# Optimization experiments

Hardware: AMD Instinct MI355X
Metric: run time of the kernel (lower is better)

Reference implementation:

```python
import jax, jax.numpy as jnp
import numpy as np

B, QN, D_IN = 2, 2048, 1024
NDS = QN // 2
HEADS, DIM_HEAD = 16, 64
INNER = HEADS * DIM_HEAD  # 1024
D_OUT = 1024


def setup_inputs() -> dict:
    key = jax.random.key(0)
    ks = jax.random.split(key, 7)
    s = 0.02
    return {
        "unet_full": jax.random.normal(ks[0], (B, QN, D_IN), jnp.float32),
        "unet_downsampled": jax.random.normal(ks[1], (B, NDS, D_IN), jnp.float32),
        "Wq": jax.random.normal(ks[2], (D_IN, INNER), jnp.float32) * s,
        "Wk": jax.random.normal(ks[3], (D_IN, INNER), jnp.float32) * s,
        "Wv": jax.random.normal(ks[4], (D_IN, INNER), jnp.float32) * s,
        "Wo": jax.random.normal(ks[5], (INNER, D_OUT), jnp.float32) * s,
        "bo": jnp.zeros((D_OUT,), jnp.float32),
    }


def reference(unet_full, unet_downsampled, Wq, Wk, Wv, Wo, bo):
    # projections
    q = unet_full @ Wq                      # [B, QN, H*D]
    k = unet_downsampled @ Wk               # [B, NDS, H*D]
    v = unet_downsampled @ Wv
    # repeat kv along sequence dim (torch repeat(1,2,1) == tile twice on dim 1)
    k = jnp.concatenate([k, k], axis=1)     # [B, KVN=2*NDS, H*D]
    v = jnp.concatenate([v, v], axis=1)
    kvn = k.shape[1]
    # split heads
    q = q.reshape(B, QN, HEADS, DIM_HEAD)
    k = k.reshape(B, kvn, HEADS, DIM_HEAD)
    v = v.reshape(B, kvn, HEADS, DIM_HEAD)
    # banded mask: triu(diagonal=-2) keeps entries where j >= i - 2; log -> 0 allowed, -inf blocked
    i = jnp.arange(QN)[:, None]
    j = jnp.arange(kvn)[None, :]
    bias = jnp.where(j >= i - 2, 0.0, -jnp.inf).astype(q.dtype)  # [QN, KVN]
    scale = 1.0 / jnp.sqrt(jnp.asarray(DIM_HEAD, q.dtype))
    scores = jnp.einsum('bqhd,bkhd->bhqk', q, k) * scale + bias[None, None]
    attn = jax.nn.softmax(scores, axis=-1)
    out = jnp.einsum('bhqk,bkhd->bqhd', attn, v)  # [B, QN, H, D]
    out = out.reshape(B, QN, INNER)
    return out @ Wo + bo
```

## Files before the change

kernel.cpp:

```cpp
#include <hip/hip_runtime.h>

typedef __attribute__((ext_vector_type(8))) short short8;
typedef __attribute__((ext_vector_type(4))) short short4v;
typedef __attribute__((ext_vector_type(4))) float floatx4;
typedef __attribute__((ext_vector_type(4))) unsigned int uint4v;
typedef __attribute__((ext_vector_type(2))) unsigned int uint2v;

__device__ __forceinline__ unsigned short f2bf(float f) {
  unsigned u = __float_as_uint(f);
  u += 0x7FFFu + ((u >> 16) & 1u);
  return (unsigned short)(u >> 16);
}
__device__ __forceinline__ unsigned pack_bf2(float f0, float f1) {
  unsigned a = __float_as_uint(f0) + 0x8000u;
  unsigned b = __float_as_uint(f1) + 0x8000u;
  return __builtin_amdgcn_perm(b, a, 0x07060302u);
}
__device__ __forceinline__ void async16(const unsigned short* g, unsigned short* l) {
  __builtin_amdgcn_global_load_lds(
      (const __attribute__((address_space(1))) unsigned int*)g,
      (__attribute__((address_space(3))) unsigned int*)l, 16, 0, 0);
}

#define B_   2
#define QN_  2048
#define NDS_ 1024
#define H_   16
#define C_SC 0.18033688011f

__global__ __launch_bounds__(256) void prep(
    const float* __restrict__ Wq, const float* __restrict__ Wk,
    const float* __restrict__ Wv, const float* __restrict__ Wo,
    unsigned short* __restrict__ WT) {
  int bid = blockIdx.x;
  int z = bid >> 8, tile = bid & 255;
  const float* W = z == 0 ? Wq : z == 1 ? Wk : z == 2 ? Wv : Wo;
  unsigned short* out = WT + (size_t)z * (1u << 20);
  __shared__ unsigned short tilebuf[64][65];
  int bi = tile >> 4, bj = tile & 15;
  int c = threadIdx.x & 63, r0 = threadIdx.x >> 6;
#pragma unroll
  for (int i = 0; i < 64; i += 4)
    tilebuf[r0 + i][c] = f2bf(W[(size_t)(bi * 64 + r0 + i) * 1024 + bj * 64 + c]);
  __syncthreads();
#pragma unroll
  for (int i = 0; i < 64; i += 4)
    out[(size_t)(bj * 64 + r0 + i) * 1024 + bi * 64 + c] = tilebuf[c][r0 + i];
}

__global__ __launch_bounds__(512) void gemm_qkv(
    const float* __restrict__ full, const float* __restrict__ ds,
    const unsigned short* __restrict__ WT,
    unsigned short* __restrict__ Qb, unsigned short* __restrict__ Kb,
    unsigned short* __restrict__ Vt) {
  __shared__ __align__(16) unsigned short As[128 * 64];
  __shared__ __align__(16) unsigned short Bs[128 * 64];
  int t = threadIdx.x;
  int lane = t & 63, wave = t >> 6;
  int lrow = lane & 15, quad = lane >> 4;
  int by = blockIdx.x;
  int colBase = blockIdx.y * 128;
  int wr = (wave & 3) * 32, wc = (wave >> 2) * 64;
  int sw = lrow & 7;

  int sel = (by < 32) ? 0 : (by < 48 ? 1 : 2);
  const unsigned short* Wt = WT + (size_t)sel * (1u << 20);
  const float* Afp = (sel == 0) ? full : ds;
  size_t arow0 = (sel == 0) ? (size_t)by * 128
                            : (size_t)(by - (sel == 1 ? 32 : 48)) * 128;

  floatx4 acc[2][4];
#pragma unroll
  for (int mi = 0; mi < 2; ++mi)
#pragma unroll
    for (int ni = 0; ni < 4; ++ni) acc[mi][ni] = (floatx4){0.f, 0.f, 0.f, 0.f};

  for (int k0 = 0; k0 < 1024; k0 += 64) {
    __syncthreads();
#pragma unroll
    for (int it = 0; it < 2; ++it) {
      int linear = it * 512 + t;
      int row = linear >> 3;
      int cg = (linear & 7) ^ (row & 7);
      const float* p = Afp + (arow0 + row) * 1024 + k0 + cg * 8;
      floatx4 x = *(const floatx4*)p, y = *(const floatx4*)(p + 4);
      uint4v u = {pack_bf2(x[0], x[1]), pack_bf2(x[2], x[3]),
                  pack_bf2(y[0], y[1]), pack_bf2(y[2], y[3])};
      *(uint4v*)&As[linear * 8] = u;
      async16(Wt + (size_t)(colBase + row) * 1024 + k0 + cg * 8, Bs + linear * 8);
    }
    __syncthreads();

#pragma unroll
    for (int ks = 0; ks < 2; ++ks) {
      int fc = ((ks * 4 + quad) ^ sw) * 8;
      short8 af[2], bfr[4];
#pragma unroll
      for (int mi = 0; mi < 2; ++mi)
        af[mi] = *(const short8*)&As[(wr + mi * 16 + lrow) * 64 + fc];
#pragma unroll
      for (int ni = 0; ni < 4; ++ni)
        bfr[ni] = *(const short8*)&Bs[(wc + ni * 16 + lrow) * 64 + fc];
#pragma unroll
      for (int mi = 0; mi < 2; ++mi)
#pragma unroll
        for (int ni = 0; ni < 4; ++ni)
          acc[mi][ni] =
              __builtin_amdgcn_mfma_f32_16x16x32_bf16(af[mi], bfr[ni], acc[mi][ni], 0, 0, 0);
    }
  }

#pragma unroll
  for (int mi = 0; mi < 2; ++mi)
#pragma unroll
    for (int ni = 0; ni < 4; ++ni) {
      int col = colBase + wc + ni * 16 + lrow;
      if (sel == 2) {
        size_t r0g = arow0 + wr + mi * 16 + quad * 4;
        size_t b = r0g >> 10, kv = r0g & 1023;
        short4v pk;
#pragma unroll
        for (int r = 0; r < 4; ++r) pk[r] = (short)f2bf(acc[mi][ni][r]);
        *(short4v*)&Vt[b * (1u << 20) + (size_t)col * 1024 + kv] = pk;
      } else {
        unsigned short* C = (sel == 0) ? Qb : Kb;
#pragma unroll
        for (int r = 0; r < 4; ++r) {
          size_t row = arow0 + wr + mi * 16 + quad * 4 + r;
          C[row * 1024 + col] = f2bf(acc[mi][ni][r]);
        }
      }
    }
}

#define PSTR 40
__global__ __launch_bounds__(512) void attn_kernel(
    const unsigned short* __restrict__ Q,
    const unsigned short* __restrict__ K,
    const unsigned short* __restrict__ V,
    unsigned short* __restrict__ O) {
  __shared__ __align__(16) unsigned short Ks[2][32 * 64];
  __shared__ __align__(16) unsigned short Vs[2][64 * 32];
  __shared__ __align__(16) unsigned short Pl[8][16 * PSTR];
  int t = threadIdx.x, lane = t & 63, wave = t >> 6;
  int lrow = lane & 15, quad = lane >> 4;
  int bh = blockIdx.y, b = bh >> 4, h = bh & 15;
  int q0 = blockIdx.x * 128, qtile = q0 + wave * 16;
  int swk = lrow & 7, swv = (lrow >> 1) & 3;

  const unsigned short* qp =
      Q + (size_t)(b * QN_ + qtile + lrow) * 1024 + h * 64 + quad * 8;
  short8 qb0 = *(const short8*)qp;
  short8 qb1 = *(const short8*)(qp + 32);

  int ts = t & 255;
  int krow = ts >> 3, kq = (ts & 7) ^ (krow & 7);
  const unsigned short* ksrc =
      K + (size_t)(b * NDS_ + krow) * 1024 + h * 64 + kq * 8;
  int vrow = ts >> 2, vq = (ts & 3) ^ ((vrow >> 1) & 3);
  const unsigned short* vsrc =
      V + ((size_t)b * 1024 + h * 64 + vrow) * 1024 + vq * 8;

  int c0 = (q0 >= 1058) ? (((q0 - 1058) >> 5) + 1) : 0;
  if (t < 256) async16(ksrc + (size_t)c0 * 32 * 1024, &Ks[0][ts * 8]);
  else         async16(vsrc + c0 * 32, &Vs[0][ts * 8]);
  const unsigned short* kpre = ksrc + (size_t)(c0 + 1) * 32 * 1024;
  const unsigned short* vpre = vsrc + (c0 + 1) * 32;

  floatx4 acc_o[4];
#pragma unroll
  for (int dt = 0; dt < 4; ++dt) acc_o[dt] = (floatx4){0.f, 0.f, 0.f, 0.f};
  float den0 = 0.f, den1 = 0.f;
  int t1 = qtile + lrow - 2, t2 = qtile + lrow - 1026;
  unsigned short* P = Pl[wave];
  int buf = 0;

  for (int c = c0; c < 32; ++c) {
    __syncthreads();
    if (c + 1 < 32) {
      if (t < 256) async16(kpre, &Ks[buf ^ 1][ts * 8]);
      else         async16(vpre, &Vs[buf ^ 1][ts * 8]);
      kpre += 32 * 1024;
      vpre += 32;
    }
    int cb = c * 32;
    bool fast2 = (cb >= qtile + 13);
    bool fast1 = (cb <= qtile - 34) && (cb >= qtile - 1011);
    if (fast1 || fast2) {
      float bias = fast2 ? 1.f : 0.f;
#pragma unroll
      for (int nt = 0; nt < 2; ++nt) {
        const unsigned short* kb = &Ks[buf][(nt * 16 + lrow) * 64];
        short8 ka0 = *(const short8*)(kb + (quad ^ swk) * 8);
        short8 ka1 = *(const short8*)(kb + ((quad + 4) ^ swk) * 8);
        floatx4 z = (floatx4){0.f, 0.f, 0.f, 0.f};
        z = __builtin_amdgcn_mfma_f32_16x16x32_bf16(ka0, qb0, z, 0, 0, 0);
        z = __builtin_amdgcn_mfma_f32_16x16x32_bf16(ka1, qb1, z, 0, 0, 0);
        float p[4];
#pragma unroll
        for (int r = 0; r < 4; ++r) {
          p[r] = __builtin_amdgcn_exp2f(fmaf(z[r], C_SC, bias));
          if (nt == 0) den0 += p[r]; else den1 += p[r];
        }
        uint2v pw = {pack_bf2(p[0], p[1]), pack_bf2(p[2], p[3])};
        *(uint2v*)&P[lrow * PSTR + nt * 16 + quad * 4] = pw;
      }
    } else {
#pragma unroll
      for (int nt = 0; nt < 2; ++nt) {
        const unsigned short* kb = &Ks[buf][(nt * 16 + lrow) * 64];
        short8 ka0 = *(const short8*)(kb + (quad ^ swk) * 8);
        short8 ka1 = *(const short8*)(kb + ((quad + 4) ^ swk) * 8);
        floatx4 z = (floatx4){0.f, 0.f, 0.f, 0.f};
        z = __builtin_amdgcn_mfma_f32_16x16x32_bf16(ka0, qb0, z, 0, 0, 0);
        z = __builtin_amdgcn_mfma_f32_16x16x32_bf16(ka1, qb1, z, 0, 0, 0);
        float p[4];
#pragma unroll
        for (int r = 0; r < 4; ++r) {
          int j0 = cb + nt * 16 + quad * 4 + r;
          float m = (j0 >= t1 ? 1.f : 0.f) + (j0 >= t2 ? 1.f : 0.f);
          p[r] = m * __builtin_amdgcn_exp2f(z[r] * C_SC);
          if (nt == 0) den0 += p[r]; else den1 += p[r];
        }
        uint2v pw = {pack_bf2(p[0], p[1]), pack_bf2(p[2], p[3])};
        *(uint2v*)&P[lrow * PSTR + nt * 16 + quad * 4] = pw;
      }
    }
    short8 pa = *(const short8*)&P[lrow * PSTR + quad * 8];
#pragma unroll
    for (int dt = 0; dt < 4; ++dt) {
      short8 vf =
          *(const short8*)&Vs[buf][(dt * 16 + lrow) * 32 + (quad ^ swv) * 8];
      acc_o[dt] = __builtin_amdgcn_mfma_f32_16x16x32_bf16(pa, vf, acc_o[dt], 0, 0, 0);
    }
    buf ^= 1;
  }
  float denom = den0 + den1;
  denom += __shfl_xor(denom, 16);
  denom += __shfl_xor(denom, 32);
  float dd[4];
#pragma unroll
  for (int r = 0; r < 4; ++r) dd[r] = __shfl(denom, quad * 4 + r);
#pragma unroll
  for (int dt = 0; dt < 4; ++dt)
#pragma unroll
    for (int r = 0; r < 4; ++r) {
      int i = qtile + quad * 4 + r;
      int col = h * 64 + dt * 16 + lrow;
      O[(size_t)(b * QN_ + i) * 1024 + col] = f2bf(acc_o[dt][r] / dd[r]);
    }
}

__global__ __launch_bounds__(512) void gemm_o(
    const unsigned short* __restrict__ Ab, const unsigned short* __restrict__ WoT,
    const float* __restrict__ bo, float* __restrict__ out) {
  __shared__ __align__(16) unsigned short As[64 * 64];
  __shared__ __align__(16) unsigned short Bs[128 * 64];
  int t = threadIdx.x;
  int lane = t & 63, wave = t >> 6;
  int lrow = lane & 15, quad = lane >> 4;
  size_t rowBase = (size_t)blockIdx.x * 64;
  int colBase = blockIdx.y * 128;
  int wr = (wave & 1) * 32, wc = (wave >> 1) * 32;
  int sw = lrow & 7;

  floatx4 acc[2][2];
#pragma unroll
  for (int mi = 0; mi < 2; ++mi)
#pragma unroll
    for (int ni = 0; ni < 2; ++ni) acc[mi][ni] = (floatx4){0.f, 0.f, 0.f, 0.f};

  for (int k0 = 0; k0 < 1024; k0 += 64) {
    __syncthreads();
    {
      int row = t >> 3;
      int cg = (t & 7) ^ (row & 7);
      async16(Ab + (rowBase + row) * 1024 + k0 + cg * 8, As + t * 8);
    }
#pragma unroll
    for (int it = 0; it < 2; ++it) {
      int linear = it * 512 + t;
      int row = linear >> 3;
      int cg = (linear & 7) ^ (row & 7);
      async16(WoT + (size_t)(colBase + row) * 1024 + k0 + cg * 8, Bs + linear * 8);
    }
    __syncthreads();

#pragma unroll
    for (int ks = 0; ks < 2; ++ks) {
      int fc = ((ks * 4 + quad) ^ sw) * 8;
      short8 af[2], bfr[2];
#pragma unroll
      for (int mi = 0; mi < 2; ++mi)
        af[mi] = *(const short8*)&As[(wr + mi * 16 + lrow) * 64 + fc];
#pragma unroll
      for (int ni = 0; ni < 2; ++ni)
        bfr[ni] = *(const short8*)&Bs[(wc + ni * 16 + lrow) * 64 + fc];
#pragma unroll
      for (int mi = 0; mi < 2; ++mi)
#pragma unroll
        for (int ni = 0; ni < 2; ++ni)
          acc[mi][ni] =
              __builtin_amdgcn_mfma_f32_16x16x32_bf16(af[mi], bfr[ni], acc[mi][ni], 0, 0, 0);
    }
  }

#pragma unroll
  for (int mi = 0; mi < 2; ++mi)
#pragma unroll
    for (int ni = 0; ni < 2; ++ni) {
      int col = colBase + wc + ni * 16 + lrow;
      float badd = bo[col];
#pragma unroll
      for (int r = 0; r < 4; ++r) {
        size_t row = rowBase + wr + mi * 16 + quad * 4 + r;
        out[row * 1024 + col] = acc[mi][ni][r] + badd;
      }
    }
}

extern "C" void kernel_launch(void* const* d_in, const int* in_sizes, int n_in,
                              void* d_out, int out_size, void* d_ws, size_t ws_size,
                              hipStream_t stream) {
  const float* full = (const float*)d_in[0];
  const float* ds   = (const float*)d_in[1];
  const float* Wq   = (const float*)d_in[2];
  const float* Wk   = (const float*)d_in[3];
  const float* Wv   = (const float*)d_in[4];
  const float* Wo   = (const float*)d_in[5];
  const float* bo   = (const float*)d_in[6];
  float* out = (float*)d_out;

  unsigned short* ws = (unsigned short*)d_ws;
  unsigned short* Qb  = ws;
  unsigned short* Kb  = ws + (4u << 20);
  unsigned short* Vt  = ws + (6u << 20);
  unsigned short* Ab  = ws + (8u << 20);
  unsigned short* WT  = ws + (12u << 20);
  unsigned short* WoT = WT + 3u * (1u << 20);

  prep<<<1024, 256, 0, stream>>>(Wq, Wk, Wv, Wo, WT);
  gemm_qkv<<<dim3(64, 8), 512, 0, stream>>>(full, ds, WT, Qb, Kb, Vt);
  attn_kernel<<<dim3(QN_ / 128, B_ * H_), 512, 0, stream>>>(Qb, Kb, Vt, Ab);
  gemm_o<<<dim3(64, 8), 512, 0, stream>>>(Ab, WoT, bo, out);
}
```

Baseline: 163.9 us.

## Give each attention wave two query tiles to reuse K/V fragments

The attention block drops from 8 to 4 waves, and each wave now handles 32 query rows as two 16-row subtiles. K and V fragments read from LDS are shared across both subtiles, and every thread issues both the K and V async loads. A chunk-level skip jumps past KV chunks that lie entirely in the masked region for the wave. The cost is more registers per wave and fewer waves per block, which may lower latency hiding.

```diff
diff --git a/kernel.cpp b/kernel.cpp
--- a/kernel.cpp
+++ b/kernel.cpp
@@ -134,7 +134,7 @@
 }
 
 #define PSTR 40
-__global__ __launch_bounds__(512) void attn_kernel(
+__global__ __launch_bounds__(256) void attn_kernel(
     const unsigned short* __restrict__ Q,
     const unsigned short* __restrict__ K,
     const unsigned short* __restrict__ V,
@@ -145,110 +145,129 @@
   int t = threadIdx.x, lane = t & 63, wave = t >> 6;
   int lrow = lane & 15, quad = lane >> 4;
   int bh = blockIdx.y, b = bh >> 4, h = bh & 15;
-  int q0 = blockIdx.x * 128, qtile = q0 + wave * 16;
+  int q0 = blockIdx.x * 128, qtile = q0 + wave * 32;
   int swk = lrow & 7, swv = (lrow >> 1) & 3;
 
-  const unsigned short* qp =
-      Q + (size_t)(b * QN_ + qtile + lrow) * 1024 + h * 64 + quad * 8;
-  short8 qb0 = *(const short8*)qp;
-  short8 qb1 = *(const short8*)(qp + 32);
-
-  int ts = t & 255;
-  int krow = ts >> 3, kq = (ts & 7) ^ (krow & 7);
+  short8 qb[2][2];
+#pragma unroll
+  for (int mi = 0; mi < 2; ++mi) {
+    const unsigned short* qp =
+        Q + (size_t)(b * QN_ + qtile + mi * 16 + lrow) * 1024 + h * 64 + quad * 8;
+    qb[mi][0] = *(const short8*)qp;
+    qb[mi][1] = *(const short8*)(qp + 32);
+  }
+
+  int krow = t >> 3, kq = (t & 7) ^ (krow & 7);
   const unsigned short* ksrc =
       K + (size_t)(b * NDS_ + krow) * 1024 + h * 64 + kq * 8;
-  int vrow = ts >> 2, vq = (ts & 3) ^ ((vrow >> 1) & 3);
+  int vrow = t >> 2, vq = (t & 3) ^ ((vrow >> 1) & 3);
   const unsigned short* vsrc =
       V + ((size_t)b * 1024 + h * 64 + vrow) * 1024 + vq * 8;
 
   int c0 = (q0 >= 1058) ? (((q0 - 1058) >> 5) + 1) : 0;
-  if (t < 256) async16(ksrc + (size_t)c0 * 32 * 1024, &Ks[0][ts * 8]);
-  else         async16(vsrc + c0 * 32, &Vs[0][ts * 8]);
+  async16(ksrc + (size_t)c0 * 32 * 1024, &Ks[0][t * 8]);
+  async16(vsrc + c0 * 32, &Vs[0][t * 8]);
   const unsigned short* kpre = ksrc + (size_t)(c0 + 1) * 32 * 1024;
   const unsigned short* vpre = vsrc + (c0 + 1) * 32;
 
-  floatx4 acc_o[4];
-#pragma unroll
-  for (int dt = 0; dt < 4; ++dt) acc_o[dt] = (floatx4){0.f, 0.f, 0.f, 0.f};
-  float den0 = 0.f, den1 = 0.f;
-  int t1 = qtile + lrow - 2, t2 = qtile + lrow - 1026;
-  unsigned short* P = Pl[wave];
+  floatx4 acc_o[2][4];
+#pragma unroll
+  for (int mi = 0; mi < 2; ++mi)
+#pragma unroll
+    for (int dt = 0; dt < 4; ++dt) acc_o[mi][dt] = (floatx4){0.f, 0.f, 0.f, 0.f};
+  float den[2][2] = {{0.f, 0.f}, {0.f, 0.f}};
+  unsigned short* P0 = Pl[wave * 2];
+  unsigned short* P1 = Pl[wave * 2 + 1];
   int buf = 0;
 
   for (int c = c0; c < 32; ++c) {
     __syncthreads();
     if (c + 1 < 32) {
-      if (t < 256) async16(kpre, &Ks[buf ^ 1][ts * 8]);
-      else         async16(vpre, &Vs[buf ^ 1][ts * 8]);
+      async16(kpre, &Ks[buf ^ 1][t * 8]);
+      async16(vpre, &Vs[buf ^ 1][t * 8]);
       kpre += 32 * 1024;
       vpre += 32;
     }
     int cb = c * 32;
-    bool fast2 = (cb >= qtile + 13);
-    bool fast1 = (cb <= qtile - 34) && (cb >= qtile - 1011);
-    if (fast1 || fast2) {
-      float bias = fast2 ? 1.f : 0.f;
-#pragma unroll
-      for (int nt = 0; nt < 2; ++nt) {
-        const unsigned short* kb = &Ks[buf][(nt * 16 + lrow) * 64];
-        short8 ka0 = *(const short8*)(kb + (quad ^ swk) * 8);
-        short8 ka1 = *(const short8*)(kb + ((quad + 4) ^ swk) * 8);
-        floatx4 z = (floatx4){0.f, 0.f, 0.f, 0.f};
-        z = __builtin_amdgcn_mfma_f32_16x16x32_bf16(ka0, qb0, z, 0, 0, 0);
-        z = __builtin_amdgcn_mfma_f32_16x16x32_bf16(ka1, qb1, z, 0, 0, 0);
-        float p[4];
-#pragma unroll
-        for (int r = 0; r < 4; ++r) {
-          p[r] = __builtin_amdgcn_exp2f(fmaf(z[r], C_SC, bias));
-          if (nt == 0) den0 += p[r]; else den1 += p[r];
+    if (cb + 31 >= qtile - 1026) {
+#pragma unroll
+      for (int mi = 0; mi < 2; ++mi) {
+        int qm = qtile + mi * 16;
+        unsigned short* P = mi ? P1 : P0;
+        bool fast2 = (cb >= qm + 13);
+        bool fast1 = (cb <= qm - 34) && (cb >= qm - 1011);
+        if (fast1 || fast2) {
+          float bias = fast2 ? 1.f : 0.f;
+#pragma unroll
+          for (int nt = 0; nt < 2; ++nt) {
+            const unsigned short* kb = &Ks[buf][(nt * 16 + lrow) * 64];
+            short8 ka0 = *(const short8*)(kb + (quad ^ swk) * 8);
+            short8 ka1 = *(const short8*)(kb + ((quad + 4) ^ swk) * 8);
+            floatx4 z = (floatx4){0.f, 0.f, 0.f, 0.f};
+            z = __builtin_amdgcn_mfma_f32_16x16x32_bf16(ka0, qb[mi][0], z, 0, 0, 0);
+            z = __builtin_amdgcn_mfma_f32_16x16x32_bf16(ka1, qb[mi][1], z, 0, 0, 0);
+            float p[4];
+#pragma unroll
+            for (int r = 0; r < 4; ++r) {
+              p[r] = __builtin_amdgcn_exp2f(fmaf(z[r], C_SC, bias));
+              den[mi][nt] += p[r];
+            }
+            uint2v pw = {pack_bf2(p[0], p[1]), pack_bf2(p[2], p[3])};
+            *(uint2v*)&P[lrow * PSTR + nt * 16 + quad * 4] = pw;
+          }
+        } else {
+          int t1 = qm + lrow - 2, t2 = qm + lrow - 1026;
+#pragma unroll
+          for (int nt = 0; nt < 2; ++nt) {
+            const unsigned short* kb = &Ks[buf][(nt * 16 + lrow) * 64];
+            short8 ka0 = *(const short8*)(kb + (quad ^ swk) * 8);
+            short8 ka1 = *(const short8*)(kb + ((quad + 4) ^ swk) * 8);
+            floatx4 z = (floatx4){0.f, 0.f, 0.f, 0.f};
+            z = __builtin_amdgcn_mfma_f32_16x16x32_bf16(ka0, qb[mi][0], z, 0, 0, 0);
+            z = __builtin_amdgcn_mfma_f32_16x16x32_bf16(ka1, qb[mi][1], z, 0, 0, 0);
+            float p[4];
+#pragma unroll
+            for (int r = 0; r < 4; ++r) {
+              int j0 = cb + nt * 16 + quad * 4 + r;
+              float m = (j0 >= t1 ? 1.f : 0.f) + (j0 >= t2 ? 1.f : 0.f);
+              p[r] = m * __builtin_amdgcn_exp2f(z[r] * C_SC);
+              den[mi][nt] += p[r];
+            }
+            uint2v pw = {pack_bf2(p[0], p[1]), pack_bf2(p[2], p[3])};
+            *(uint2v*)&P[lrow * PSTR + nt * 16 + quad * 4] = pw;
+          }
         }
-        uint2v pw = {pack_bf2(p[0], p[1]), pack_bf2(p[2], p[3])};
-        *(uint2v*)&P[lrow * PSTR + nt * 16 + quad * 4] = pw;
-      }
-    } else {
-#pragma unroll
-      for (int nt = 0; nt < 2; ++nt) {
-        const unsigned short* kb = &Ks[buf][(nt * 16 + lrow) * 64];
-        short8 ka0 = *(const short8*)(kb + (quad ^ swk) * 8);
-        short8 ka1 = *(const short8*)(kb + ((quad + 4) ^ swk) * 8);
-        floatx4 z = (floatx4){0.f, 0.f, 0.f, 0.f};
-        z = __builtin_amdgcn_mfma_f32_16x16x32_bf16(ka0, qb0, z, 0, 0, 0);
-        z = __builtin_amdgcn_mfma_f32_16x16x32_bf16(ka1, qb1, z, 0, 0, 0);
-        float p[4];
-#pragma unroll
-        for (int r = 0; r < 4; ++r) {
-          int j0 = cb + nt * 16 + quad * 4 + r;
-          float m = (j0 >= t1 ? 1.f : 0.f) + (j0 >= t2 ? 1.f : 0.f);
-          p[r] = m * __builtin_amdgcn_exp2f(z[r] * C_SC);
-          if (nt == 0) den0 += p[r]; else den1 += p[r];
-        }
-        uint2v pw = {pack_bf2(p[0], p[1]), pack_bf2(p[2], p[3])};
-        *(uint2v*)&P[lrow * PSTR + nt * 16 + quad * 4] = pw;
-      }
-    }
-    short8 pa = *(const short8*)&P[lrow * PSTR + quad * 8];
-#pragma unroll
-    for (int dt = 0; dt < 4; ++dt) {
-      short8 vf =
-          *(const short8*)&Vs[buf][(dt * 16 + lrow) * 32 + (quad ^ swv) * 8];
-      acc_o[dt] = __builtin_amdgcn_mfma_f32_16x16x32_bf16(pa, vf, acc_o[dt], 0, 0, 0);
+      }
+      short8 pa0 = *(const short8*)&P0[lrow * PSTR + quad * 8];
+      short8 pa1 = *(const short8*)&P1[lrow * PSTR + quad * 8];
+#pragma unroll
+      for (int dt = 0; dt < 4; ++dt) {
+        short8 vf =
+            *(const short8*)&Vs[buf][(dt * 16 + lrow) * 32 + (quad ^ swv) * 8];
+        acc_o[0][dt] = __builtin_amdgcn_mfma_f32_16x16x32_bf16(pa0, vf, acc_o[0][dt], 0, 0, 0);
+        acc_o[1][dt] = __builtin_amdgcn_mfma_f32_16x16x32_bf16(pa1, vf, acc_o[1][dt], 0, 0, 0);
+      }
     }
     buf ^= 1;
   }
-  float denom = den0 + den1;
-  denom += __shfl_xor(denom, 16);
-  denom += __shfl_xor(denom, 32);
-  float dd[4];
-#pragma unroll
-  for (int r = 0; r < 4; ++r) dd[r] = __shfl(denom, quad * 4 + r);
-#pragma unroll
-  for (int dt = 0; dt < 4; ++dt)
-#pragma unroll
-    for (int r = 0; r < 4; ++r) {
-      int i = qtile + quad * 4 + r;
-      int col = h * 64 + dt * 16 + lrow;
-      O[(size_t)(b * QN_ + i) * 1024 + col] = f2bf(acc_o[dt][r] / dd[r]);
-    }
+
+#pragma unroll
+  for (int mi = 0; mi < 2; ++mi) {
+    float denom = den[mi][0] + den[mi][1];
+    denom += __shfl_xor(denom, 16);
+    denom += __shfl_xor(denom, 32);
+    float dd[4];
+#pragma unroll
+    for (int r = 0; r < 4; ++r) dd[r] = __shfl(denom, quad * 4 + r);
+#pragma unroll
+    for (int dt = 0; dt < 4; ++dt)
+#pragma unroll
+      for (int r = 0; r < 4; ++r) {
+        int i = qtile + mi * 16 + quad * 4 + r;
+        int col = h * 64 + dt * 16 + lrow;
+        O[(size_t)(b * QN_ + i) * 1024 + col] = f2bf(acc_o[mi][dt][r] / dd[r]);
+      }
+  }
 }
 
 __global__ __launch_bounds__(512) void gemm_o(
@@ -341,6 +360,6 @@
 
   prep<<<1024, 256, 0, stream>>>(Wq, Wk, Wv, Wo, WT);
   gemm_qkv<<<dim3(64, 8), 512, 0, stream>>>(full, ds, WT, Qb, Kb, Vt);
-  attn_kernel<<<dim3(QN_ / 128, B_ * H_), 512, 0, stream>>>(Qb, Kb, Vt, Ab);
+  attn_kernel<<<dim3(QN_ / 128, B_ * H_), 256, 0, stream>>>(Qb, Kb, Vt, Ab);
   gemm_o<<<dim3(64, 8), 512, 0, stream>>>(Ab, WoT, bo, out);
 }
```

After: 180.7 us. +10.3%, slower.

## Load K/V fragments directly from global memory per wave, dropping LDS staging

Applied to the files above, without the earlier changes.

The attention kernel no longer stages K and V tiles in double-buffered shared memory with async loads and block-wide barriers. Each wave now reads its MFMA operands straight from global memory, relying on L1/L2 for reuse across the 8 waves. Each wave also computes its own starting chunk, so waves skip masked chunks independently. This removes the __syncthreads per chunk and the LDS traffic, but gives up the explicit prefetch and means eight redundant global loads per tile, which depends on cache hit rates.

```diff
diff --git a/kernel.cpp b/kernel.cpp
--- a/kernel.cpp
+++ b/kernel.cpp
@@ -139,33 +139,20 @@
     const unsigned short* __restrict__ K,
     const unsigned short* __restrict__ V,
     unsigned short* __restrict__ O) {
-  __shared__ __align__(16) unsigned short Ks[2][32 * 64];
-  __shared__ __align__(16) unsigned short Vs[2][64 * 32];
   __shared__ __align__(16) unsigned short Pl[8][16 * PSTR];
   int t = threadIdx.x, lane = t & 63, wave = t >> 6;
   int lrow = lane & 15, quad = lane >> 4;
   int bh = blockIdx.y, b = bh >> 4, h = bh & 15;
   int q0 = blockIdx.x * 128, qtile = q0 + wave * 16;
-  int swk = lrow & 7, swv = (lrow >> 1) & 3;
 
   const unsigned short* qp =
       Q + (size_t)(b * QN_ + qtile + lrow) * 1024 + h * 64 + quad * 8;
   short8 qb0 = *(const short8*)qp;
   short8 qb1 = *(const short8*)(qp + 32);
 
-  int ts = t & 255;
-  int krow = ts >> 3, kq = (ts & 7) ^ (krow & 7);
-  const unsigned short* ksrc =
-      K + (size_t)(b * NDS_ + krow) * 1024 + h * 64 + kq * 8;
-  int vrow = ts >> 2, vq = (ts & 3) ^ ((vrow >> 1) & 3);
-  const unsigned short* vsrc =
-      V + ((size_t)b * 1024 + h * 64 + vrow) * 1024 + vq * 8;
-
-  int c0 = (q0 >= 1058) ? (((q0 - 1058) >> 5) + 1) : 0;
-  if (t < 256) async16(ksrc + (size_t)c0 * 32 * 1024, &Ks[0][ts * 8]);
-  else         async16(vsrc + c0 * 32, &Vs[0][ts * 8]);
-  const unsigned short* kpre = ksrc + (size_t)(c0 + 1) * 32 * 1024;
-  const unsigned short* vpre = vsrc + (c0 + 1) * 32;
+  const unsigned short* Kb0 = K + (size_t)b * NDS_ * 1024 + h * 64 + quad * 8;
+  const unsigned short* Vb0 =
+      V + ((size_t)b * 1024 + h * 64 + lrow) * 1024 + quad * 8;
 
   floatx4 acc_o[4];
 #pragma unroll
@@ -173,16 +160,10 @@
   float den0 = 0.f, den1 = 0.f;
   int t1 = qtile + lrow - 2, t2 = qtile + lrow - 1026;
   unsigned short* P = Pl[wave];
-  int buf = 0;
-
-  for (int c = c0; c < 32; ++c) {
-    __syncthreads();
-    if (c + 1 < 32) {
-      if (t < 256) async16(kpre, &Ks[buf ^ 1][ts * 8]);
-      else         async16(vpre, &Vs[buf ^ 1][ts * 8]);
-      kpre += 32 * 1024;
-      vpre += 32;
-    }
+
+  int c0w = (qtile >= 1058) ? (((qtile - 1058) >> 5) + 1) : 0;
+
+  for (int c = c0w; c < 32; ++c) {
     int cb = c * 32;
     bool fast2 = (cb >= qtile + 13);
     bool fast1 = (cb <= qtile - 34) && (cb >= qtile - 1011);
@@ -190,9 +171,9 @@
       float bias = fast2 ? 1.f : 0.f;
 #pragma unroll
       for (int nt = 0; nt < 2; ++nt) {
-        const unsigned short* kb = &Ks[buf][(nt * 16 + lrow) * 64];
-        short8 ka0 = *(const short8*)(kb + (quad ^ swk) * 8);
-        short8 ka1 = *(const short8*)(kb + ((quad + 4) ^ swk) * 8);
+        const unsigned short* kr = Kb0 + (size_t)(cb + nt * 16 + lrow) * 1024;
+        short8 ka0 = *(const short8*)kr;
+        short8 ka1 = *(const short8*)(kr + 32);
         floatx4 z = (floatx4){0.f, 0.f, 0.f, 0.f};
         z = __builtin_amdgcn_mfma_f32_16x16x32_bf16(ka0, qb0, z, 0, 0, 0);
         z = __builtin_amdgcn_mfma_f32_16x16x32_bf16(ka1, qb1, z, 0, 0, 0);
@@ -208,9 +189,9 @@
     } else {
 #pragma unroll
       for (int nt = 0; nt < 2; ++nt) {
-        const unsigned short* kb = &Ks[buf][(nt * 16 + lrow) * 64];
-        short8 ka0 = *(const short8*)(kb + (quad ^ swk) * 8);
-        short8 ka1 = *(const short8*)(kb + ((quad + 4) ^ swk) * 8);
+        const unsigned short* kr = Kb0 + (size_t)(cb + nt * 16 + lrow) * 1024;
+        short8 ka0 = *(const short8*)kr;
+        short8 ka1 = *(const short8*)(kr + 32);
         floatx4 z = (floatx4){0.f, 0.f, 0.f, 0.f};
         z = __builtin_amdgcn_mfma_f32_16x16x32_bf16(ka0, qb0, z, 0, 0, 0);
         z = __builtin_amdgcn_mfma_f32_16x16x32_bf16(ka1, qb1, z, 0, 0, 0);
@@ -229,11 +210,9 @@
     short8 pa = *(const short8*)&P[lrow * PSTR + quad * 8];
 #pragma unroll
     for (int dt = 0; dt < 4; ++dt) {
-      short8 vf =
-          *(const short8*)&Vs[buf][(dt * 16 + lrow) * 32 + (quad ^ swv) * 8];
+      short8 vf = *(const short8*)(Vb0 + (size_t)(dt * 16) * 1024 + cb);
       acc_o[dt] = __builtin_amdgcn_mfma_f32_16x16x32_bf16(pa, vf, acc_o[dt], 0, 0, 0);
     }
-    buf ^= 1;
   }
   float denom = den0 + den1;
   denom += __shfl_xor(denom, 16);
```

Result: slower. 251.5 us (+53.5%).
